# Optimization experiments

Measured on AMD Instinct MI355X. Metric: run time of the kernel, lower is better.

Reference implementation:

```python
import jax, jax.numpy as jnp
import numpy as np

B, C, H, W = 32, 512, 32, 32
HID, MEM = 256, 256


def setup_inputs() -> dict:
    key = jax.random.key(0)
    k1, k2, k3, k4, k5, k6 = jax.random.split(key, 6)
    x = jax.random.normal(k1, (B, C, H, W), dtype=jnp.float32)
    h = jax.random.normal(k2, (B, MEM), dtype=jnp.float32)
    # conv1: 1x1 conv, no bias -> weight [HID, C]
    W_conv1 = jax.random.normal(k3, (HID, C), dtype=jnp.float32) / np.sqrt(C)
    # linear1: memory_dim -> hidden_dim, with bias
    W_lin = jax.random.normal(k4, (HID, MEM), dtype=jnp.float32) / np.sqrt(MEM)
    b_lin = jax.random.normal(k5, (HID,), dtype=jnp.float32) * 0.01
    # attention_conv: 1x1 conv hidden->1, no bias -> weight [HID]
    W_attn = jax.random.normal(k6, (HID,), dtype=jnp.float32) / np.sqrt(HID)
    return {"x": x, "h": h, "W_conv1": W_conv1, "W_lin": W_lin,
            "b_lin": b_lin, "W_attn": W_attn}


def reference(x, h, W_conv1, W_lin, b_lin, W_attn):
    # x: [B,C,H,W], h: [B,MEM]
    x2 = x.reshape(x.shape[0], x.shape[1], -1)            # [B,C,HW]
    x3 = jnp.einsum('bchw,kc->bkhw', x, W_conv1)          # 1x1 conv -> [B,HID,H,W]
    h3 = (h @ W_lin.T + b_lin)[:, :, None, None]          # [B,HID,1,1] broadcast over H,W
    a1 = jnp.tanh(x3 + h3)                                # [B,HID,H,W]
    a2 = jnp.einsum('bkhw,k->bhw', a1, W_attn).reshape(x.shape[0], -1)  # [B,HW]
    a3 = jax.nn.softmax(a2, axis=1)                       # [B,HW]
    context = jnp.einsum('bcs,bs->bc', x2, a3)            # [B,C]
    return (a3, context)
```

## Files before the change

### kernel.cpp

```cpp
#include <hip/hip_runtime.h>
#include <hip/hip_bf16.h>
#include <cmath>


typedef __bf16 bf16;
typedef __attribute__((ext_vector_type(8))) __bf16 bf16x8;
typedef __attribute__((ext_vector_type(4))) float f32x4;

__global__ __launch_bounds__(256) void prep_kernel(const float* __restrict__ h,
                                                   const float* __restrict__ Wlin,
                                                   const float* __restrict__ blin,
                                                   const float* __restrict__ Wc,
                                                   float* __restrict__ h3,
                                                   bf16* __restrict__ Whi,
                                                   bf16* __restrict__ Wlo) {
    const int tid = threadIdx.x;
    if (blockIdx.x < 32) {
        const int b = blockIdx.x;
        __shared__ float hs[256];
        hs[tid] = h[b * 256 + tid];
        __syncthreads();
        const float4* wr = (const float4*)(Wlin + (size_t)tid * 256);
        float acc = blin[tid];
        #pragma unroll 8
        for (int q = 0; q < 64; ++q) {
            float4 w = wr[q];
            float4 hv = *(const float4*)&hs[q * 4];
            acc = fmaf(w.x, hv.x, fmaf(w.y, hv.y, fmaf(w.z, hv.z, fmaf(w.w, hv.w, acc))));
        }
        h3[b * 256 + tid] = acc;
    } else {
        const int e0 = (blockIdx.x - 32) * 2048 + tid * 8;
        float4 v0 = *(const float4*)(Wc + e0);
        float4 v1 = *(const float4*)(Wc + e0 + 4);
        float vs[8] = {v0.x, v0.y, v0.z, v0.w, v1.x, v1.y, v1.z, v1.w};
        bf16x8 vh, vl;
        #pragma unroll
        for (int j = 0; j < 8; ++j) {
            bf16 hi = (bf16)vs[j];
            float r = vs[j] - (float)hi;
            vh[j] = hi;
            vl[j] = (bf16)r;
        }
        *(bf16x8*)&Whi[e0] = vh;
        *(bf16x8*)&Wlo[e0] = vl;
    }
}

__global__ __launch_bounds__(256, 3) void fused_mfma(const float* __restrict__ x,
                                                     const bf16* __restrict__ Whi,
                                                     const bf16* __restrict__ Wlo,
                                                     const float* __restrict__ h3,
                                                     const float* __restrict__ Wattn,
                                                     float* __restrict__ a2) {
    __shared__ bf16 Ahi[128 * 64];
    __shared__ bf16 Alo[128 * 64];
    __shared__ bf16 Bhi[64 * 64];
    __shared__ bf16 Blo[64 * 64];
    __shared__ float red2[4 * 64];

    const int tid = threadIdx.x;
    const int bid = blockIdx.x;
    const int wk = (bid & 7) * 128 + (bid >> 3);
    const int b  = wk >> 5;
    const int st = (wk >> 1) & 15;
    const int mb = wk & 1;
    const int s0 = st * 64;
    const int r0 = mb * 128;

    const int w  = tid >> 6;
    const int l  = tid & 63;
    const int g  = l >> 4;
    const int lr = l & 15;

    const float* xb = x + ((size_t)b << 19);

    f32x4 acc[2][4];
    #pragma unroll
    for (int mf = 0; mf < 2; ++mf)
        #pragma unroll
        for (int nf = 0; nf < 4; ++nf)
            acc[mf][nf] = (f32x4){0.f, 0.f, 0.f, 0.f};

    const int arow_ = tid >> 3;
    const int acol  = (tid & 7) * 8;
    const int bs    = (tid >> 3) * 2;
    const int bc_   = (tid & 7) * 2;

    #pragma unroll 1
    for (int c0 = 0; c0 < 512; c0 += 64) {
        bf16x8 wva[4], wvl[4];
        #pragma unroll
        for (int jj = 0; jj < 4; ++jj) {
            int row = arow_ + 32 * jj;
            size_t off = (size_t)(r0 + row) * 512 + c0 + acol;
            wva[jj] = *(const bf16x8*)(Whi + off);
            wvl[jj] = *(const bf16x8*)(Wlo + off);
        }
        float2 xv0[4], xv1[4];
        #pragma unroll
        for (int jj = 0; jj < 4; ++jj) {
            int cc = bc_ + 16 * jj;
            xv0[jj] = *(const float2*)(xb + (size_t)(c0 + cc) * 1024 + s0 + bs);
            xv1[jj] = *(const float2*)(xb + (size_t)(c0 + cc + 1) * 1024 + s0 + bs);
        }
        __syncthreads();
        #pragma unroll
        for (int jj = 0; jj < 4; ++jj) {
            int row = arow_ + 32 * jj;
            int idx = row * 64 + (acol ^ (8 * (row & 7)));
            *(bf16x8*)&Ahi[idx] = wva[jj];
            *(bf16x8*)&Alo[idx] = wvl[jj];
        }
        #pragma unroll
        for (int jj = 0; jj < 4; ++jj) {
            int cc = bc_ + 16 * jj;
            bf16 h00 = (bf16)xv0[jj].x, h10 = (bf16)xv1[jj].x;
            bf16 h01 = (bf16)xv0[jj].y, h11 = (bf16)xv1[jj].y;
            bf16 l00 = (bf16)(xv0[jj].x - (float)h00), l10 = (bf16)(xv1[jj].x - (float)h10);
            bf16 l01 = (bf16)(xv0[jj].y - (float)h01), l11 = (bf16)(xv1[jj].y - (float)h11);
            int i0 = bs * 64 + (cc ^ (8 * (bs & 7)));
            int i1 = (bs + 1) * 64 + (cc ^ (8 * ((bs + 1) & 7)));
            Bhi[i0] = h00; Bhi[i0 + 1] = h10;
            Blo[i0] = l00; Blo[i0 + 1] = l10;
            Bhi[i1] = h01; Bhi[i1 + 1] = h11;
            Blo[i1] = l01; Blo[i1 + 1] = l11;
        }
        __syncthreads();
        #pragma unroll
        for (int kk = 0; kk < 2; ++kk) {
            bf16x8 ah[2], al[2], bh[4], bl[4];
            #pragma unroll
            for (int mf = 0; mf < 2; ++mf) {
                int row = w * 32 + mf * 16 + lr;
                int idx = row * 64 + ((kk * 32 + 8 * g) ^ (8 * (row & 7)));
                ah[mf] = *(const bf16x8*)&Ahi[idx];
                al[mf] = *(const bf16x8*)&Alo[idx];
            }
            #pragma unroll
            for (int nf = 0; nf < 4; ++nf) {
                int srow = nf * 16 + lr;
                int idx = srow * 64 + ((kk * 32 + 8 * g) ^ (8 * (srow & 7)));
                bh[nf] = *(const bf16x8*)&Bhi[idx];
                bl[nf] = *(const bf16x8*)&Blo[idx];
            }
            #pragma unroll
            for (int mf = 0; mf < 2; ++mf)
                #pragma unroll
                for (int nf = 0; nf < 4; ++nf) {
                    acc[mf][nf] = __builtin_amdgcn_mfma_f32_16x16x32_bf16(ah[mf], bh[nf], acc[mf][nf], 0, 0, 0);
                    acc[mf][nf] = __builtin_amdgcn_mfma_f32_16x16x32_bf16(ah[mf], bl[nf], acc[mf][nf], 0, 0, 0);
                    acc[mf][nf] = __builtin_amdgcn_mfma_f32_16x16x32_bf16(al[mf], bh[nf], acc[mf][nf], 0, 0, 0);
                }
        }
    }

    const float* h3b = h3 + b * 256;
    float part[4] = {0.f, 0.f, 0.f, 0.f};
    #pragma unroll
    for (int mf = 0; mf < 2; ++mf) {
        #pragma unroll
        for (int i = 0; i < 4; ++i) {
            int kch = r0 + w * 32 + mf * 16 + g * 4 + i;
            float hv = h3b[kch];
            float wt = Wattn[kch];
            #pragma unroll
            for (int nf = 0; nf < 4; ++nf)
                part[nf] += wt * tanhf(acc[mf][nf][i] + hv);
        }
    }
    #pragma unroll
    for (int nf = 0; nf < 4; ++nf) {
        part[nf] += __shfl_xor(part[nf], 16, 64);
        part[nf] += __shfl_xor(part[nf], 32, 64);
    }
    if (l < 16) {
        #pragma unroll
        for (int nf = 0; nf < 4; ++nf) red2[w * 64 + nf * 16 + l] = part[nf];
    }
    __syncthreads();
    if (tid < 64) {
        float tot = red2[tid] + red2[64 + tid] + red2[128 + tid] + red2[192 + tid];
        atomicAdd(&a2[(size_t)b * 1024 + s0 + tid], tot);
    }
}

__global__ __launch_bounds__(256) void softmax_context(const float* __restrict__ x,
                                                       const float* __restrict__ a2,
                                                       float* __restrict__ a3,
                                                       float* __restrict__ ctx) {
    __shared__ float sm[1024];
    __shared__ float red[8];
    const int tid = threadIdx.x;
    const int b = blockIdx.y, ct = blockIdx.x;
    const int wave = tid >> 6, lane = tid & 63;

    float4 v = ((const float4*)(a2 + (size_t)b * 1024))[tid];
    float m = fmaxf(fmaxf(v.x, v.y), fmaxf(v.z, v.w));
    #pragma unroll
    for (int off = 32; off >= 1; off >>= 1) m = fmaxf(m, __shfl_xor(m, off, 64));
    if (lane == 0) red[wave] = m;
    __syncthreads();
    m = fmaxf(fmaxf(red[0], red[1]), fmaxf(red[2], red[3]));
    float e0 = expf(v.x - m), e1 = expf(v.y - m), e2 = expf(v.z - m), e3 = expf(v.w - m);
    float s = e0 + e1 + e2 + e3;
    #pragma unroll
    for (int off = 32; off >= 1; off >>= 1) s += __shfl_xor(s, off, 64);
    if (lane == 0) red[4 + wave] = s;
    __syncthreads();
    s = red[4] + red[5] + red[6] + red[7];
    float inv = 1.f / s;
    float4 o = {e0 * inv, e1 * inv, e2 * inv, e3 * inv};
    ((float4*)sm)[tid] = o;
    if (ct == 0) ((float4*)(a3 + (size_t)b * 1024))[tid] = o;
    __syncthreads();

    const float* xb = x + ((size_t)b << 19);
    #pragma unroll
    for (int r = 0; r < 8; ++r) {
        int c = ct * 32 + wave * 8 + r;
        const float4* row = (const float4*)(xb + (size_t)c * 1024);
        float sum = 0.f;
        #pragma unroll
        for (int it = 0; it < 4; ++it) {
            int idx = it * 64 + lane;
            float4 xv = row[idx];
            float4 av = *(const float4*)&sm[idx * 4];
            sum = fmaf(xv.x, av.x, fmaf(xv.y, av.y, fmaf(xv.z, av.z, fmaf(xv.w, av.w, sum))));
        }
        #pragma unroll
        for (int off = 32; off >= 1; off >>= 1) sum += __shfl_xor(sum, off, 64);
        if (lane == 0) ctx[(size_t)b * 512 + c] = sum;
    }
}

extern "C" void kernel_launch(void* const* d_in, const int* in_sizes, int n_in,
                              void* d_out, int out_size, void* d_ws, size_t ws_size,
                              hipStream_t stream) {
    const float* x     = (const float*)d_in[0];
    const float* h     = (const float*)d_in[1];
    const float* Wc    = (const float*)d_in[2];
    const float* Wlin  = (const float*)d_in[3];
    const float* blin  = (const float*)d_in[4];
    const float* Wattn = (const float*)d_in[5];

    float* out = (float*)d_out;
    float* a3  = out;
    float* ctx = out + 32 * 1024;

    char* ws = (char*)d_ws;
    float* h3 = (float*)ws;
    float* a2 = (float*)(ws + 32768);
    bf16* Whi = (bf16*)(ws + 32768 + 131072);
    bf16* Wlo = (bf16*)(ws + 32768 + 131072 + 262144);

    hipMemsetAsync(a2, 0, 32 * 1024 * sizeof(float), stream);
    hipLaunchKernelGGL(prep_kernel, dim3(96), dim3(256), 0, stream, h, Wlin, blin, Wc, h3, Whi, Wlo);
    hipLaunchKernelGGL(fused_mfma, dim3(1024), dim3(256), 0, stream, x, Whi, Wlo, h3, Wattn, a2);
    hipLaunchKernelGGL(softmax_context, dim3(16, 32), dim3(256), 0, stream, x, a2, a3, ctx);
}
```

Before: 162.7 us.

## Prefetch next K-tile into registers, vectorize B staging, fold memset, widen context grid

The GEMM main loop now loads the next 64-channel slice of weights and x into registers after the barrier, so global latency overlaps the MFMA work on the current tile. x is loaded as float4 along the spatial dimension, and the hi/lo bf16 split is written to LDS as bf16x4 vectors instead of scalar stores. The a2 memset is folded into prep_kernel, which removes one launch. The softmax/context grid is doubled with fewer channels per block, which raises parallelism but also repeats the softmax work in each extra block.

```diff
diff --git a/kernel.cpp b/kernel.cpp
--- a/kernel.cpp
+++ b/kernel.cpp
@@ -5,6 +5,7 @@
 
 typedef __bf16 bf16;
 typedef __attribute__((ext_vector_type(8))) __bf16 bf16x8;
+typedef __attribute__((ext_vector_type(4))) __bf16 bf16x4;
 typedef __attribute__((ext_vector_type(4))) float f32x4;
 
 __global__ __launch_bounds__(256) void prep_kernel(const float* __restrict__ h,
@@ -13,7 +14,8 @@
                                                    const float* __restrict__ Wc,
                                                    float* __restrict__ h3,
                                                    bf16* __restrict__ Whi,
-                                                   bf16* __restrict__ Wlo) {
+                                                   bf16* __restrict__ Wlo,
+                                                   float* __restrict__ a2) {
     const int tid = threadIdx.x;
     if (blockIdx.x < 32) {
         const int b = blockIdx.x;
@@ -44,6 +46,8 @@
         }
         *(bf16x8*)&Whi[e0] = vh;
         *(bf16x8*)&Wlo[e0] = vl;
+        float2 z = {0.f, 0.f};
+        *(float2*)&a2[(blockIdx.x - 32) * 512 + tid * 2] = z;
     }
 }
 
@@ -84,26 +88,25 @@
 
     const int arow_ = tid >> 3;
     const int acol  = (tid & 7) * 8;
-    const int bs    = (tid >> 3) * 2;
-    const int bc_   = (tid & 7) * 2;
+    const int sp = (tid & 15) * 4;
+    const int cb = (tid >> 4) * 4;
+
+    bf16x8 wva[4], wvl[4];
+    float4 xv[4];
+
+    #pragma unroll
+    for (int jj = 0; jj < 4; ++jj) {
+        int row = arow_ + 32 * jj;
+        size_t off = (size_t)(r0 + row) * 512 + acol;
+        wva[jj] = *(const bf16x8*)(Whi + off);
+        wvl[jj] = *(const bf16x8*)(Wlo + off);
+    }
+    #pragma unroll
+    for (int jj = 0; jj < 4; ++jj)
+        xv[jj] = *(const float4*)(xb + (size_t)(cb + jj) * 1024 + s0 + sp);
 
     #pragma unroll 1
     for (int c0 = 0; c0 < 512; c0 += 64) {
-        bf16x8 wva[4], wvl[4];
-        #pragma unroll
-        for (int jj = 0; jj < 4; ++jj) {
-            int row = arow_ + 32 * jj;
-            size_t off = (size_t)(r0 + row) * 512 + c0 + acol;
-            wva[jj] = *(const bf16x8*)(Whi + off);
-            wvl[jj] = *(const bf16x8*)(Wlo + off);
-        }
-        float2 xv0[4], xv1[4];
-        #pragma unroll
-        for (int jj = 0; jj < 4; ++jj) {
-            int cc = bc_ + 16 * jj;
-            xv0[jj] = *(const float2*)(xb + (size_t)(c0 + cc) * 1024 + s0 + bs);
-            xv1[jj] = *(const float2*)(xb + (size_t)(c0 + cc + 1) * 1024 + s0 + bs);
-        }
         __syncthreads();
         #pragma unroll
         for (int jj = 0; jj < 4; ++jj) {
@@ -112,21 +115,41 @@
             *(bf16x8*)&Ahi[idx] = wva[jj];
             *(bf16x8*)&Alo[idx] = wvl[jj];
         }
-        #pragma unroll
-        for (int jj = 0; jj < 4; ++jj) {
-            int cc = bc_ + 16 * jj;
-            bf16 h00 = (bf16)xv0[jj].x, h10 = (bf16)xv1[jj].x;
-            bf16 h01 = (bf16)xv0[jj].y, h11 = (bf16)xv1[jj].y;
-            bf16 l00 = (bf16)(xv0[jj].x - (float)h00), l10 = (bf16)(xv1[jj].x - (float)h10);
-            bf16 l01 = (bf16)(xv0[jj].y - (float)h01), l11 = (bf16)(xv1[jj].y - (float)h11);
-            int i0 = bs * 64 + (cc ^ (8 * (bs & 7)));
-            int i1 = (bs + 1) * 64 + (cc ^ (8 * ((bs + 1) & 7)));
-            Bhi[i0] = h00; Bhi[i0 + 1] = h10;
-            Blo[i0] = l00; Blo[i0 + 1] = l10;
-            Bhi[i1] = h01; Bhi[i1 + 1] = h11;
-            Blo[i1] = l01; Blo[i1 + 1] = l11;
+        {
+            bf16 hi[4][4], lo[4][4];
+            #pragma unroll
+            for (int jj = 0; jj < 4; ++jj) {
+                float vv[4] = {xv[jj].x, xv[jj].y, xv[jj].z, xv[jj].w};
+                #pragma unroll
+                for (int ss = 0; ss < 4; ++ss) {
+                    bf16 hh = (bf16)vv[ss];
+                    hi[jj][ss] = hh;
+                    lo[jj][ss] = (bf16)(vv[ss] - (float)hh);
+                }
+            }
+            #pragma unroll
+            for (int ss = 0; ss < 4; ++ss) {
+                int row = sp + ss;
+                int idx = row * 64 + (cb ^ (8 * (row & 7)));
+                bf16x4 ph = {hi[0][ss], hi[1][ss], hi[2][ss], hi[3][ss]};
+                bf16x4 pl = {lo[0][ss], lo[1][ss], lo[2][ss], lo[3][ss]};
+                *(bf16x4*)&Bhi[idx] = ph;
+                *(bf16x4*)&Blo[idx] = pl;
+            }
         }
         __syncthreads();
+        if (c0 + 64 < 512) {
+            #pragma unroll
+            for (int jj = 0; jj < 4; ++jj) {
+                int row = arow_ + 32 * jj;
+                size_t off = (size_t)(r0 + row) * 512 + (c0 + 64) + acol;
+                wva[jj] = *(const bf16x8*)(Whi + off);
+                wvl[jj] = *(const bf16x8*)(Wlo + off);
+            }
+            #pragma unroll
+            for (int jj = 0; jj < 4; ++jj)
+                xv[jj] = *(const float4*)(xb + (size_t)(c0 + 64 + cb + jj) * 1024 + s0 + sp);
+        }
         #pragma unroll
         for (int kk = 0; kk < 2; ++kk) {
             bf16x8 ah[2], al[2], bh[4], bl[4];
@@ -217,8 +240,8 @@
 
     const float* xb = x + ((size_t)b << 19);
     #pragma unroll
-    for (int r = 0; r < 8; ++r) {
-        int c = ct * 32 + wave * 8 + r;
+    for (int r = 0; r < 4; ++r) {
+        int c = ct * 16 + wave * 4 + r;
         const float4* row = (const float4*)(xb + (size_t)c * 1024);
         float sum = 0.f;
         #pragma unroll
@@ -254,8 +277,7 @@
     bf16* Whi = (bf16*)(ws + 32768 + 131072);
     bf16* Wlo = (bf16*)(ws + 32768 + 131072 + 262144);
 
-    hipMemsetAsync(a2, 0, 32 * 1024 * sizeof(float), stream);
-    hipLaunchKernelGGL(prep_kernel, dim3(96), dim3(256), 0, stream, h, Wlin, blin, Wc, h3, Whi, Wlo);
+    hipLaunchKernelGGL(prep_kernel, dim3(96), dim3(256), 0, stream, h, Wlin, blin, Wc, h3, Whi, Wlo, a2);
     hipLaunchKernelGGL(fused_mfma, dim3(1024), dim3(256), 0, stream, x, Whi, Wlo, h3, Wattn, a2);
-    hipLaunchKernelGGL(softmax_context, dim3(16, 32), dim3(256), 0, stream, x, a2, a3, ctx);
-}
+    hipLaunchKernelGGL(softmax_context, dim3(32, 32), dim3(256), 0, stream, x, a2, a3, ctx);
+}
```

Result: faster. 149.9 us (-7.9%).
